# Performance work log

Hardware: AMD Instinct MI355X
Metric: run time of the kernel (lower is better)

## Reference

```python
import jax, jax.numpy as jnp
import numpy as np

N_HEAD, D_HEAD, D_MODEL = 8, 64, 512
QLEN, MLEN, BSZ = 1024, 1024, 4
KLEN = QLEN + MLEN
SCALE = 1.0 / (D_HEAD ** 0.5)
LN_EPS = 1e-5


def _rel_shift(x):
    # x: [qlen, rlen, bsz, n_head]
    q, rl, b, n = x.shape
    zero_pad = jnp.zeros((q, 1, b, n), x.dtype)
    x_padded = jnp.concatenate([zero_pad, x], axis=1).reshape(rl + 1, q, b, n)
    return x_padded[1:].reshape(q, rl, b, n)


def _layer_norm(x, g, b):
    mu = jnp.mean(x, axis=-1, keepdims=True)
    var = jnp.var(x, axis=-1, keepdims=True)
    return (x - mu) * jax.lax.rsqrt(var + LN_EPS) * g + b


def setup_inputs() -> dict:
    key = jax.random.key(0)
    ks = jax.random.split(key, 10)
    s = 0.02
    return {
        "w": jax.random.normal(ks[0], (QLEN, BSZ, D_MODEL), jnp.float32),
        "r": jax.random.normal(ks[1], (KLEN, 1, D_MODEL), jnp.float32),
        "r_w_bias": jax.random.normal(ks[2], (N_HEAD, D_HEAD), jnp.float32) * s,
        "r_r_bias": jax.random.normal(ks[3], (N_HEAD, D_HEAD), jnp.float32) * s,
        "mems": jax.random.normal(ks[4], (MLEN, BSZ, D_MODEL), jnp.float32),
        "Wq": jax.random.normal(ks[5], (D_MODEL, N_HEAD * D_HEAD), jnp.float32) * s,
        "Wkv": jax.random.normal(ks[6], (D_MODEL, 2 * N_HEAD * D_HEAD), jnp.float32) * s,
        "Wr": jax.random.normal(ks[7], (D_MODEL, N_HEAD * D_HEAD), jnp.float32) * s,
        "Wo": jax.random.normal(ks[8], (N_HEAD * D_HEAD, D_MODEL), jnp.float32) * s,
        "ln_g": jnp.ones((D_MODEL,), jnp.float32),
        "ln_b": jnp.zeros((D_MODEL,), jnp.float32),
        # causal mask: query i can attend keys j <= i + MLEN
        "attn_mask": jnp.arange(KLEN)[None, :] > (jnp.arange(QLEN) + MLEN)[:, None],
    }


def reference(w, r, r_w_bias, r_r_bias, mems, Wq, Wkv, Wr, Wo, ln_g, ln_b, attn_mask):
    qlen, bsz = w.shape[0], w.shape[1]
    cat = jnp.concatenate([mems, w], axis=0)          # [klen, bsz, d_model]
    klen = cat.shape[0]

    r_head_k = (r[:, 0] @ Wr).reshape(-1, N_HEAD, D_HEAD)   # [rlen, n, d]
    kv = cat @ Wkv                                           # [klen, bsz, 2*n*d]
    w_head_k, w_head_v = jnp.split(kv, 2, axis=-1)
    w_head_q = (cat[-qlen:] @ Wq).reshape(qlen, bsz, N_HEAD, D_HEAD)
    w_head_k = w_head_k.reshape(klen, bsz, N_HEAD, D_HEAD)
    w_head_v = w_head_v.reshape(klen, bsz, N_HEAD, D_HEAD)

    AC = jnp.einsum('ibnd,jbnd->ijbn', w_head_q + r_w_bias, w_head_k)
    BD = jnp.einsum('ibnd,jnd->ijbn', w_head_q + r_r_bias, r_head_k)
    BD = _rel_shift(BD)[:, :klen]

    attn_score = (AC + BD) * SCALE                           # [qlen, klen, bsz, n]
    attn_score = jnp.where(attn_mask[:, :, None, None], -jnp.inf, attn_score)
    attn_prob = jax.nn.softmax(attn_score, axis=1)

    attn_vec = jnp.einsum('ijbn,jbnd->ibnd', attn_prob, w_head_v)
    attn_vec = attn_vec.reshape(qlen, bsz, N_HEAD * D_HEAD)
    attn_out = attn_vec @ Wo
    return _layer_norm(w + attn_out, ln_g, ln_b)
```

## Files before the change

### kernel.cpp

```cpp
#include <hip/hip_runtime.h>
#include <hip/hip_bf16.h>
#include <math.h>

#define QLEN 1024
#define MLEN 1024
#define KLEN 2048
#define BSZ 4
#define NH 8
#define DH 64
#define DM 512
#define SCALE 0.125f
#define LN_EPS 1e-5f

#define RK_ROWS 2176
#define D2STR 36

typedef __attribute__((ext_vector_type(8))) short short8;
typedef __attribute__((ext_vector_type(4))) float float4_;

__device__ inline ushort to_bf16(float x) {
  __hip_bfloat16 h = __float2bfloat16(x);
  return *reinterpret_cast<ushort*>(&h);
}
__device__ inline float bf16_to_f(ushort u) {
  union { unsigned int i; float f; } v;
  v.i = (unsigned int)u << 16;
  return v.f;
}

__device__ inline float row_max16(float v) {
  int x = __builtin_bit_cast(int, v);
  v = fmaxf(v, __builtin_bit_cast(float, __builtin_amdgcn_update_dpp(x, x, 0xB1, 0xF, 0xF, false)));
  x = __builtin_bit_cast(int, v);
  v = fmaxf(v, __builtin_bit_cast(float, __builtin_amdgcn_update_dpp(x, x, 0x4E, 0xF, 0xF, false)));
  x = __builtin_bit_cast(int, v);
  v = fmaxf(v, __builtin_bit_cast(float, __builtin_amdgcn_update_dpp(x, x, 0x124, 0xF, 0xF, false)));
  x = __builtin_bit_cast(int, v);
  v = fmaxf(v, __builtin_bit_cast(float, __builtin_amdgcn_update_dpp(x, x, 0x128, 0xF, 0xF, false)));
  return v;
}
__device__ inline float row_sum16(float v) {
  int x = __builtin_bit_cast(int, v);
  v += __builtin_bit_cast(float, __builtin_amdgcn_update_dpp(x, x, 0xB1, 0xF, 0xF, false));
  x = __builtin_bit_cast(int, v);
  v += __builtin_bit_cast(float, __builtin_amdgcn_update_dpp(x, x, 0x4E, 0xF, 0xF, false));
  x = __builtin_bit_cast(int, v);
  v += __builtin_bit_cast(float, __builtin_amdgcn_update_dpp(x, x, 0x124, 0xF, 0xF, false));
  x = __builtin_bit_cast(int, v);
  v += __builtin_bit_cast(float, __builtin_amdgcn_update_dpp(x, x, 0x128, 0xF, 0xF, false));
  return v;
}

__global__ __launch_bounds__(256) void wtrans_all(
    const float* __restrict__ Wq, const float* __restrict__ Wkv,
    const float* __restrict__ Wr, const float* __restrict__ Wo,
    ushort* __restrict__ WqT, ushort* __restrict__ WkvT,
    ushort* __restrict__ WrT, ushort* __restrict__ WoT) {
  __shared__ ushort tile[32][33];
  const int z = blockIdx.z;
  const float* W;
  ushort* WT;
  int N;
  if (z == 0)      { W = Wq;  WT = WqT;  N = DM; }
  else if (z == 1) { W = Wkv; WT = WkvT; N = 2 * DM; }
  else if (z == 2) { W = Wr;  WT = WrT;  N = DM; }
  else             { W = Wo;  WT = WoT;  N = DM; }
  const int k0 = blockIdx.x * 32, n0 = blockIdx.y * 32;
  if (n0 >= N) return;
  const int tid = threadIdx.x;
#pragma unroll
  for (int it = 0; it < 4; ++it) {
    int idx = tid + it * 256;
    int r = idx >> 5, c = idx & 31;
    tile[r][c] = to_bf16(W[(size_t)(k0 + r) * N + n0 + c]);
  }
  __syncthreads();
#pragma unroll
  for (int it = 0; it < 4; ++it) {
    int idx = tid + it * 256;
    int r = idx >> 5, c = idx & 31;
    WT[(size_t)(n0 + r) * DM + k0 + c] = tile[c][r];
  }
}

__global__ __launch_bounds__(256) void proj_all(
    const float* __restrict__ w, const float* __restrict__ mems,
    const float* __restrict__ r,
    const ushort* __restrict__ WqT, const ushort* __restrict__ WkvT,
    const ushort* __restrict__ WrT,
    const float* __restrict__ bias0, const float* __restrict__ bias1,
    ushort* __restrict__ qw, ushort* __restrict__ qr,
    ushort* __restrict__ k2, ushort* __restrict__ v2,
    ushort* __restrict__ rk2) {
  __shared__ ushort As[128 * 32];
  __shared__ ushort Bs[128 * 32];
  const int tid = threadIdx.x;
  int mode, bx, by;
  {
    int id = blockIdx.x;
    if (id < 128)      { mode = 0; bx = id >> 2;         by = id & 3; }
    else if (id < 640) { mode = 1; bx = (id - 128) >> 3; by = (id - 128) & 7; }
    else               { mode = 2; bx = (id - 640) >> 2; by = (id - 640) & 3; }
  }
  const int m0 = bx * 128, n0 = by * 128;
  const int wv = tid >> 6, lane = tid & 63;
  const int wm = wv >> 1, wn = wv & 1;
  const int l16 = lane & 15, quad = lane >> 4;

  const int arow = tid >> 1;
  const int acol = (tid & 1) * 16;
  const float* asrc;
  {
    int m = m0 + arow;
    if (mode == 2) asrc = r + (size_t)m * DM;
    else asrc = (m < QLEN * BSZ) ? w + (size_t)m * DM
                                 : mems + (size_t)(m - QLEN * BSZ) * DM;
    asrc += acol;
  }
  const ushort* BT = (mode == 0) ? WqT : (mode == 1) ? WkvT : WrT;
  const ushort* bsrc = BT + (size_t)(n0 + arow) * DM + acol;

  float4_ acc[4][4];
#pragma unroll
  for (int a = 0; a < 4; ++a)
#pragma unroll
    for (int b = 0; b < 4; ++b) acc[a][b] = float4_{0.f, 0.f, 0.f, 0.f};

  for (int k0 = 0; k0 < DM; k0 += 32) {
    float4 a0 = *reinterpret_cast<const float4*>(asrc + k0);
    float4 a1 = *reinterpret_cast<const float4*>(asrc + k0 + 4);
    float4 a2 = *reinterpret_cast<const float4*>(asrc + k0 + 8);
    float4 a3 = *reinterpret_cast<const float4*>(asrc + k0 + 12);
    ushort4 u0, u1, u2, u3;
    u0.x = to_bf16(a0.x); u0.y = to_bf16(a0.y); u0.z = to_bf16(a0.z); u0.w = to_bf16(a0.w);
    u1.x = to_bf16(a1.x); u1.y = to_bf16(a1.y); u1.z = to_bf16(a1.z); u1.w = to_bf16(a1.w);
    u2.x = to_bf16(a2.x); u2.y = to_bf16(a2.y); u2.z = to_bf16(a2.z); u2.w = to_bf16(a2.w);
    u3.x = to_bf16(a3.x); u3.y = to_bf16(a3.y); u3.z = to_bf16(a3.z); u3.w = to_bf16(a3.w);
    *reinterpret_cast<ushort4*>(&As[arow * 32 + acol]) = u0;
    *reinterpret_cast<ushort4*>(&As[arow * 32 + acol + 4]) = u1;
    *reinterpret_cast<ushort4*>(&As[arow * 32 + acol + 8]) = u2;
    *reinterpret_cast<ushort4*>(&As[arow * 32 + acol + 12]) = u3;
    *reinterpret_cast<uint4*>(&Bs[arow * 32 + acol]) =
        *reinterpret_cast<const uint4*>(bsrc + k0);
    *reinterpret_cast<uint4*>(&Bs[arow * 32 + acol + 8]) =
        *reinterpret_cast<const uint4*>(bsrc + k0 + 8);
    __syncthreads();
    short8 af[4], bf[4];
#pragma unroll
    for (int f = 0; f < 4; ++f) {
      af[f] = *reinterpret_cast<const short8*>(&As[(wm * 64 + f * 16 + l16) * 32 + quad * 8]);
      bf[f] = *reinterpret_cast<const short8*>(&Bs[(wn * 64 + f * 16 + l16) * 32 + quad * 8]);
    }
#pragma unroll
    for (int fm = 0; fm < 4; ++fm)
#pragma unroll
      for (int fn = 0; fn < 4; ++fn)
        acc[fm][fn] = __builtin_amdgcn_mfma_f32_16x16x32_bf16(bf[fn], af[fm], acc[fm][fn], 0, 0, 0);
    __syncthreads();
  }

#pragma unroll
  for (int fm = 0; fm < 4; ++fm) {
#pragma unroll
    for (int fn = 0; fn < 4; ++fn) {
      const int mm = m0 + wm * 64 + fm * 16 + l16;
      const int nnb = n0 + wn * 64 + fn * 16 + quad * 4;
      const float4_ a = acc[fm][fn];
      if (mode == 0) {
        float4 b0v = *reinterpret_cast<const float4*>(bias0 + nnb);
        float4 b1v = *reinterpret_cast<const float4*>(bias1 + nnb);
        int i = mm >> 2, b = mm & 3;
        int hd = nnb >> 6, d0 = nnb & 63;
        size_t idx = (((size_t)(b * NH + hd)) * QLEN + i) * DH + d0;
        ushort4 o0, o1;
        o0.x = to_bf16(a[0] + b0v.x); o0.y = to_bf16(a[1] + b0v.y);
        o0.z = to_bf16(a[2] + b0v.z); o0.w = to_bf16(a[3] + b0v.w);
        o1.x = to_bf16(a[0] + b1v.x); o1.y = to_bf16(a[1] + b1v.y);
        o1.z = to_bf16(a[2] + b1v.z); o1.w = to_bf16(a[3] + b1v.w);
        *reinterpret_cast<ushort4*>(qw + idx) = o0;
        *reinterpret_cast<ushort4*>(qr + idx) = o1;
      } else if (mode == 1) {
        int pos = mm >> 2, b = mm & 3;
        if (nnb < DM) {
          int jb = pos >> 5, jj = pos & 31;
          int hd = nnb >> 6, d = nnb & 63;
          int bn = b * NH + hd;
          int tile = ((jj >> 4) << 1) | (d >> 5);
          int lane2 = (((d >> 3) & 3) << 4) | (jj & 15);
          ushort4 o;
          o.x = to_bf16(a[0]); o.y = to_bf16(a[1]);
          o.z = to_bf16(a[2]); o.w = to_bf16(a[3]);
          *reinterpret_cast<ushort4*>(
              k2 + ((((size_t)bn * 64 + jb) * 4 + tile) * 64 + lane2) * 8 + (d & 7)) = o;
        } else {
          int nn2 = nnb - DM;
          int hd = nn2 >> 6, dbase = nn2 & 63;
          int bn = b * NH + hd;
          int jb64 = pos >> 6, j64 = pos & 63;
          int s_g = (j64 & 15) * 4 + (j64 >> 4);
          int half = s_g >> 5, s_ = s_g & 31;
          size_t flat = (((size_t)bn * 32 + jb64) * 8 + (dbase >> 4) * 2 + half) * 512
                      + (size_t)((s_ >> 3) * 16 + (dbase & 15)) * 8 + (s_ & 7);
#pragma unroll
          for (int reg = 0; reg < 4; ++reg)
            v2[flat + (size_t)reg * 8] = to_bf16(a[reg]);
        }
      } else {
        int t = mm;
        int hd = nnb >> 6, d = nnb & 63;
        ushort4 o;
        o.x = to_bf16(a[0]); o.y = to_bf16(a[1]);
        o.z = to_bf16(a[2]); o.w = to_bf16(a[3]);
        *reinterpret_cast<ushort4*>(
            rk2 + ((size_t)hd * RK_ROWS + t) * DH + d) = o;
      }
    }
  }
}

__device__ inline uint4 combine8(uint4 u0, uint4 u1, float s0, float s1) {
  union U { uint4 v; ushort u[8]; };
  U a, b, o;
  a.v = u0; b.v = u1;
#pragma unroll
  for (int e = 0; e < 8; ++e)
    o.u[e] = to_bf16(bf16_to_f(a.u[e]) * s0 + bf16_to_f(b.u[e]) * s1);
  return o.v;
}

__global__ __launch_bounds__(256) void mfma_out(
    const ushort* __restrict__ O0, const ushort* __restrict__ O1,
    const float* __restrict__ ml, const ushort* __restrict__ BT,
    float* __restrict__ Y) {
  __shared__ ushort As[128 * 32];
  __shared__ ushort Bs[128 * 32];
  const int tid = threadIdx.x;
  const int m0 = blockIdx.x * 128, n0 = blockIdx.y * 128;
  const int wv = tid >> 6, lane = tid & 63;
  const int wm = wv >> 1, wn = wv & 1;
  const int l16 = lane & 15, quad = lane >> 4;
  const int arow = tid >> 1;
  const int acol = (tid & 1) * 16;
  const int row = m0 + arow;
  const ushort* bsrc = BT + (size_t)(n0 + arow) * DM + acol;
  const float2* mlp = (const float2*)ml;

  float4_ acc[4][4];
#pragma unroll
  for (int a = 0; a < 4; ++a)
#pragma unroll
    for (int b = 0; b < 4; ++b) acc[a][b] = float4_{0.f, 0.f, 0.f, 0.f};

  for (int k0 = 0; k0 < DM; k0 += 32) {
    const int col0 = k0 + acol;
    const int h = col0 >> 6;
    float2 a = mlp[(size_t)row * NH + h];
    float2 c = mlp[(size_t)(QLEN * BSZ + row) * NH + h];
    float M = fmaxf(a.x, c.x);
    float e0 = __builtin_amdgcn_exp2f(a.x - M);
    float e1 = __builtin_amdgcn_exp2f(c.x - M);
    float inv = 1.f / (a.y * e0 + c.y * e1);
    float s0 = e0 * inv, s1 = e1 * inv;
    size_t ob = (size_t)row * DM + col0;
    uint4 u0a = *reinterpret_cast<const uint4*>(O0 + ob);
    uint4 u0b = *reinterpret_cast<const uint4*>(O0 + ob + 8);
    uint4 u1a = *reinterpret_cast<const uint4*>(O1 + ob);
    uint4 u1b = *reinterpret_cast<const uint4*>(O1 + ob + 8);
    *reinterpret_cast<uint4*>(&As[arow * 32 + acol]) = combine8(u0a, u1a, s0, s1);
    *reinterpret_cast<uint4*>(&As[arow * 32 + acol + 8]) = combine8(u0b, u1b, s0, s1);
    *reinterpret_cast<uint4*>(&Bs[arow * 32 + acol]) = *reinterpret_cast<const uint4*>(bsrc + k0);
    *reinterpret_cast<uint4*>(&Bs[arow * 32 + acol + 8]) = *reinterpret_cast<const uint4*>(bsrc + k0 + 8);
    __syncthreads();
    short8 af[4], bf[4];
#pragma unroll
    for (int f = 0; f < 4; ++f) {
      af[f] = *reinterpret_cast<const short8*>(&As[(wm * 64 + f * 16 + l16) * 32 + quad * 8]);
      bf[f] = *reinterpret_cast<const short8*>(&Bs[(wn * 64 + f * 16 + l16) * 32 + quad * 8]);
    }
#pragma unroll
    for (int fm = 0; fm < 4; ++fm)
#pragma unroll
      for (int fn = 0; fn < 4; ++fn)
        acc[fm][fn] = __builtin_amdgcn_mfma_f32_16x16x32_bf16(bf[fn], af[fm], acc[fm][fn], 0, 0, 0);
    __syncthreads();
  }
#pragma unroll
  for (int fm = 0; fm < 4; ++fm)
#pragma unroll
    for (int fn = 0; fn < 4; ++fn) {
      int mm = m0 + wm * 64 + fm * 16 + l16;
      int nnb = n0 + wn * 64 + fn * 16 + quad * 4;
      float4 o;
      o.x = acc[fm][fn][0]; o.y = acc[fm][fn][1];
      o.z = acc[fm][fn][2]; o.w = acc[fm][fn][3];
      *reinterpret_cast<float4*>(Y + (size_t)mm * DM + nnb) = o;
    }
}

__global__ __launch_bounds__(256) void ln_fuse(
    const float* __restrict__ y, const float* __restrict__ wres,
    const float* __restrict__ g, const float* __restrict__ bb,
    float* __restrict__ out) {
  const int row = blockIdx.x * 4 + (threadIdx.x >> 6);
  const int lane = threadIdx.x & 63;
  const float* yr = y + (size_t)row * DM + lane * 4;
  const float* wr = wres + (size_t)row * DM + lane * 4;
  float4 x0 = *(const float4*)yr;
  float4 x1 = *(const float4*)(yr + 256);
  float4 w0 = *(const float4*)wr;
  float4 w1 = *(const float4*)(wr + 256);
  x0.x += w0.x; x0.y += w0.y; x0.z += w0.z; x0.w += w0.w;
  x1.x += w1.x; x1.y += w1.y; x1.z += w1.z; x1.w += w1.w;
  float s = x0.x + x0.y + x0.z + x0.w + x1.x + x1.y + x1.z + x1.w;
  float ss = x0.x * x0.x + x0.y * x0.y + x0.z * x0.z + x0.w * x0.w +
             x1.x * x1.x + x1.y * x1.y + x1.z * x1.z + x1.w * x1.w;
#pragma unroll
  for (int off = 1; off <= 32; off <<= 1) {
    s += __shfl_xor(s, off, 64);
    ss += __shfl_xor(ss, off, 64);
  }
  float mu = s * (1.f / DM);
  float var = ss * (1.f / DM) - mu * mu;
  float rstd = rsqrtf(var + LN_EPS);
  float4 g0 = *(const float4*)(g + lane * 4);
  float4 g1 = *(const float4*)(g + lane * 4 + 256);
  float4 b0 = *(const float4*)(bb + lane * 4);
  float4 b1 = *(const float4*)(bb + lane * 4 + 256);
  float4 o0, o1;
  o0.x = (x0.x - mu) * rstd * g0.x + b0.x;
  o0.y = (x0.y - mu) * rstd * g0.y + b0.y;
  o0.z = (x0.z - mu) * rstd * g0.z + b0.z;
  o0.w = (x0.w - mu) * rstd * g0.w + b0.w;
  o1.x = (x1.x - mu) * rstd * g1.x + b1.x;
  o1.y = (x1.y - mu) * rstd * g1.y + b1.y;
  o1.z = (x1.z - mu) * rstd * g1.z + b1.z;
  o1.w = (x1.w - mu) * rstd * g1.w + b1.w;
  float* orow = out + (size_t)row * DM + lane * 4;
  *reinterpret_cast<float4*>(orow) = o0;
  *reinterpret_cast<float4*>(orow + 256) = o1;
}

__global__ __launch_bounds__(256, 2) void attn_mfma(
    const ushort* __restrict__ qw, const ushort* __restrict__ qr,
    const ushort* __restrict__ k2, const ushort* __restrict__ v2,
    const ushort* __restrict__ rk2, ushort* __restrict__ Opart,
    float* __restrict__ ml) {
  const int i0b = (gridDim.x - 1 - blockIdx.x) * 128;
  const int n = blockIdx.y;
  const int b = blockIdx.z >> 1, seg = blockIdx.z & 1;
  const int bn = b * NH + n;
  const int tid = threadIdx.x;
  const int wv = tid >> 6, lane = tid & 63;
  const int l16 = lane & 15, quad = lane >> 4;
  const int i0w = i0b + wv * 32;

  __shared__ float D2all[4][96 * D2STR];
  __shared__ ushort Pall[4][1024];
  float* __restrict__ Dw = D2all[wv];
  ushort* __restrict__ Pw = Pall[wv];

  const ushort* __restrict__ k2b = k2 + (size_t)bn * (64 * 4 * 512);
  const ushort* __restrict__ v2b = v2 + (size_t)bn * (32 * 8 * 512);
  const ushort* __restrict__ rk2n = rk2 + (size_t)n * RK_ROWS * DH;

  const int nIterTot = i0b / 64 + 18;
  const int nHalf = nIterTot >> 1;
  const int c0 = seg ? nHalf : 0;
  const int c1 = seg ? nIterTot : nHalf;

  short8 aqw[2][2], aqr[2][2];
#pragma unroll
  for (int g = 0; g < 2; ++g) {
    const ushort* qwp = qw + (((size_t)bn * QLEN) + i0w + g * 16 + l16) * DH + quad * 8;
    const ushort* qrp = qr + (((size_t)bn * QLEN) + i0w + g * 16 + l16) * DH + quad * 8;
    aqw[g][0] = *(const short8*)(qwp);
    aqw[g][1] = *(const short8*)(qwp + 32);
    aqr[g][0] = *(const short8*)(qrp);
    aqr[g][1] = *(const short8*)(qrp + 32);
  }

  float4_ O[2][4];
  float mrow[2][4], lpart[2][4];
#pragma unroll
  for (int g = 0; g < 2; ++g)
#pragma unroll
    for (int t = 0; t < 4; ++t) {
      O[g][t] = float4_{0.f, 0.f, 0.f, 0.f};
      mrow[g][t] = -INFINITY;
      lpart[g][t] = 0.f;
    }
  const float SL2E = SCALE * 1.44269504088896f;

  for (int k = c0; k < c1; ++k) {
    const int j0 = k * 64;

    float4_ ac[2][4];
#pragma unroll
    for (int h = 0; h < 4; ++h) {
      const ushort* kb = k2b +
          ((size_t)(k * 2 + (h >> 1)) * 4 + (h & 1) * 2) * 512 + lane * 8;
      short8 b0 = *(const short8*)(kb);
      short8 b1 = *(const short8*)(kb + 512);
#pragma unroll
      for (int g = 0; g < 2; ++g) {
        float4_ c = {0.f, 0.f, 0.f, 0.f};
        c = __builtin_amdgcn_mfma_f32_16x16x32_bf16(aqw[g][0], b0, c, 0, 0, 0);
        c = __builtin_amdgcn_mfma_f32_16x16x32_bf16(aqw[g][1], b1, c, 0, 0, 0);
        ac[g][h] = c;
      }
    }

    const int rb = j0 - i0w + 992;
#pragma unroll
    for (int tt = 0; tt < 6; ++tt) {
      const ushort* rrow = rk2n + (size_t)(rb + tt * 16 + l16) * DH;
      short8 r0 = *(const short8*)(rrow + quad * 8);
      short8 r1 = *(const short8*)(rrow + 32 + quad * 8);
      float* dst = Dw + (tt * 16 + l16) * D2STR + quad * 4;
      if (tt < 5) {
        float4_ d = {0.f, 0.f, 0.f, 0.f};
        d = __builtin_amdgcn_mfma_f32_16x16x32_bf16(aqr[1][0], r0, d, 0, 0, 0);
        d = __builtin_amdgcn_mfma_f32_16x16x32_bf16(aqr[1][1], r1, d, 0, 0, 0);
        *reinterpret_cast<float4_*>(dst + 16) = d;
      }
      if (tt > 0) {
        float4_ d = {0.f, 0.f, 0.f, 0.f};
        d = __builtin_amdgcn_mfma_f32_16x16x32_bf16(aqr[0][0], r0, d, 0, 0, 0);
        d = __builtin_amdgcn_mfma_f32_16x16x32_bf16(aqr[0][1], r1, d, 0, 0, 0);
        *reinterpret_cast<float4_*>(dst) = d;
      }
    }

    short8 pf[2][2];
#pragma unroll
    for (int g = 0; g < 2; ++g) {
      float s4[4][4];
#pragma unroll
      for (int hh = 0; hh < 4; ++hh)
#pragma unroll
        for (int rg = 0; rg < 4; ++rg) {
          int wrow = g * 16 + quad * 4 + rg;
          float bd = Dw[(hh * 16 + l16 + 31 - wrow) * D2STR + wrow];
          float sv = (ac[g][hh][rg] + bd) * SL2E;
          s4[hh][rg] = (j0 + hh * 16 + l16 > i0w + wrow + MLEN) ? -INFINITY : sv;
        }
#pragma unroll
      for (int rg = 0; rg < 4; ++rg) {
        float mx = row_max16(fmaxf(fmaxf(s4[0][rg], s4[1][rg]),
                                   fmaxf(s4[2][rg], s4[3][rg])));
        float mn = fmaxf(mrow[g][rg], mx);
        float alpha = __builtin_amdgcn_exp2f(mrow[g][rg] - mn);
        float p0 = __builtin_amdgcn_exp2f(s4[0][rg] - mn);
        float p1 = __builtin_amdgcn_exp2f(s4[1][rg] - mn);
        float p2 = __builtin_amdgcn_exp2f(s4[2][rg] - mn);
        float p3 = __builtin_amdgcn_exp2f(s4[3][rg] - mn);
        lpart[g][rg] = lpart[g][rg] * alpha + (p0 + p1 + p2 + p3);
        mrow[g][rg] = mn;
#pragma unroll
        for (int t = 0; t < 4; ++t) O[g][t][rg] *= alpha;
        unsigned int u0 = (unsigned int)to_bf16(p0) | ((unsigned int)to_bf16(p1) << 16);
        unsigned int u1 = (unsigned int)to_bf16(p2) | ((unsigned int)to_bf16(p3) << 16);
        int flat = (l16 >> 1) * 128 + (quad * 4 + rg) * 8 + (l16 & 1) * 4;
        *reinterpret_cast<uint2*>(Pw + flat) = make_uint2(u0, u1);
      }
      pf[g][0] = *(const short8*)(Pw + lane * 8);
      pf[g][1] = *(const short8*)(Pw + 512 + lane * 8);
    }

#pragma unroll
    for (int t = 0; t < 4; ++t) {
      const ushort* vb = v2b + ((size_t)k * 8 + t * 2) * 512 + lane * 8;
      short8 vf0 = *(const short8*)(vb);
      short8 vf1 = *(const short8*)(vb + 512);
#pragma unroll
      for (int g = 0; g < 2; ++g) {
        O[g][t] = __builtin_amdgcn_mfma_f32_16x16x32_bf16(pf[g][0], vf0, O[g][t], 0, 0, 0);
        O[g][t] = __builtin_amdgcn_mfma_f32_16x16x32_bf16(pf[g][1], vf1, O[g][t], 0, 0, 0);
      }
    }
  }

  ushort* op = Opart + (size_t)seg * QLEN * BSZ * DM;
  float2* mlp = (float2*)ml;
#pragma unroll
  for (int g = 0; g < 2; ++g) {
    float lsum[4];
#pragma unroll
    for (int rg = 0; rg < 4; ++rg) lsum[rg] = row_sum16(lpart[g][rg]);
#pragma unroll
    for (int rg = 0; rg < 4; ++rg) {
      int row = g * 16 + quad * 4 + rg;
      if (l16 == 0) {
        mlp[((size_t)seg * QLEN * BSZ + (size_t)(i0w + row) * BSZ + b) * NH + n] =
            float2{mrow[g][rg], lsum[rg]};
      }
#pragma unroll
      for (int t = 0; t < 4; ++t) {
        op[((size_t)(i0w + row) * BSZ + b) * DM + n * DH + t * 16 + l16] =
            to_bf16(O[g][t][rg]);
      }
    }
  }
}

extern "C" void kernel_launch(void* const* d_in, const int* in_sizes, int n_in,
                              void* d_out, int out_size, void* d_ws, size_t ws_size,
                              hipStream_t stream) {
  const float* w    = (const float*)d_in[0];
  const float* r    = (const float*)d_in[1];
  const float* rwb  = (const float*)d_in[2];
  const float* rrb  = (const float*)d_in[3];
  const float* mems = (const float*)d_in[4];
  const float* Wq   = (const float*)d_in[5];
  const float* Wkv  = (const float*)d_in[6];
  const float* Wr   = (const float*)d_in[7];
  const float* Wo   = (const float*)d_in[8];
  const float* ln_g = (const float*)d_in[9];
  const float* ln_b = (const float*)d_in[10];
  float* out = (float*)d_out;

  char* p = (char*)d_ws;
  auto alloc = [&](size_t bytes) {
    char* q = p;
    p += (bytes + 255) & ~(size_t)255;
    return q;
  };
  ushort* WqT   = (ushort*)alloc((size_t)DM * DM * 2);
  ushort* WkvT  = (ushort*)alloc((size_t)2 * DM * DM * 2);
  ushort* WrT   = (ushort*)alloc((size_t)DM * DM * 2);
  ushort* WoT   = (ushort*)alloc((size_t)DM * DM * 2);
  ushort* qw    = (ushort*)alloc((size_t)BSZ * NH * QLEN * DH * 2);
  ushort* qr    = (ushort*)alloc((size_t)BSZ * NH * QLEN * DH * 2);
  ushort* k2    = (ushort*)alloc((size_t)BSZ * NH * 64 * 4 * 512 * 2);
  ushort* v2    = (ushort*)alloc((size_t)BSZ * NH * 32 * 8 * 512 * 2);
  ushort* rk2   = (ushort*)alloc((size_t)NH * RK_ROWS * DH * 2);
  ushort* Opart = (ushort*)alloc((size_t)2 * QLEN * BSZ * DM * 2);
  float*  ml    = (float*)alloc((size_t)2 * QLEN * BSZ * NH * 2 * 4);
  float* y = (float*)k2;

  wtrans_all<<<dim3(16, 32, 4), dim3(256), 0, stream>>>(
      Wq, Wkv, Wr, Wo, WqT, WkvT, WrT, WoT);
  proj_all<<<dim3(704), dim3(256), 0, stream>>>(
      w, mems, r, WqT, WkvT, WrT, rwb, rrb, qw, qr, k2, v2, rk2);
  attn_mfma<<<dim3(QLEN / 128, NH, BSZ * 2), dim3(256), 0, stream>>>(
      qw, qr, k2, v2, rk2, Opart, ml);
  mfma_out<<<dim3(32, 4), dim3(256), 0, stream>>>(
      Opart, Opart + (size_t)QLEN * BSZ * DM, ml, WoT, y);
  ln_fuse<<<dim3(QLEN * BSZ / 4), dim3(256), 0, stream>>>(y, w, ln_g, ln_b, out);
}
```

Baseline: 258.8 us.

## Prefetch K/V fragments, store BD in bf16, swizzle P buffer, add MFMA priorities

Next-iteration K fragments are now loaded into registers while the current iteration computes, and V fragments are loaded at the start of each iteration so global latency overlaps the MFMA and softmax work. The relative-position BD scratch tile in LDS is stored as bf16 instead of fp32, which halves its LDS footprint and traffic. The P staging buffer uses an XOR-swizzled layout to reduce LDS bank conflicts. s_setprio is raised around MFMA blocks. The changes add register pressure that may hurt occupancy, and the bf16 BD scratch adds rounding error.

```diff
diff --git a/kernel.cpp b/kernel.cpp
--- a/kernel.cpp
+++ b/kernel.cpp
@@ -354,9 +354,9 @@
   const int l16 = lane & 15, quad = lane >> 4;
   const int i0w = i0b + wv * 32;
 
-  __shared__ float D2all[4][96 * D2STR];
+  __shared__ ushort D2all[4][96 * D2STR];
   __shared__ ushort Pall[4][1024];
-  float* __restrict__ Dw = D2all[wv];
+  ushort* __restrict__ Dw = D2all[wv];
   ushort* __restrict__ Pw = Pall[wv];
 
   const ushort* __restrict__ k2b = k2 + (size_t)bn * (64 * 4 * 512);
@@ -390,46 +390,78 @@
       lpart[g][t] = 0.f;
     }
   const float SL2E = SCALE * 1.44269504088896f;
+  const int px = l16 >> 1, ppar = l16 & 1;
+
+  short8 kf[8], kfN[8];
+  auto load_k = [&](int kk, short8* dst) {
+#pragma unroll
+    for (int h = 0; h < 4; ++h) {
+      const ushort* kb = k2b +
+          ((size_t)(kk * 2 + (h >> 1)) * 4 + (h & 1) * 2) * 512 + lane * 8;
+      dst[h * 2 + 0] = *(const short8*)(kb);
+      dst[h * 2 + 1] = *(const short8*)(kb + 512);
+    }
+  };
+  load_k(c0, kf);
 
   for (int k = c0; k < c1; ++k) {
     const int j0 = k * 64;
 
+    short8 vf[8];
+#pragma unroll
+    for (int t = 0; t < 4; ++t) {
+      const ushort* vb = v2b + ((size_t)k * 8 + t * 2) * 512 + lane * 8;
+      vf[t * 2 + 0] = *(const short8*)(vb);
+      vf[t * 2 + 1] = *(const short8*)(vb + 512);
+    }
+
+    __builtin_amdgcn_s_setprio(1);
     float4_ ac[2][4];
 #pragma unroll
     for (int h = 0; h < 4; ++h) {
-      const ushort* kb = k2b +
-          ((size_t)(k * 2 + (h >> 1)) * 4 + (h & 1) * 2) * 512 + lane * 8;
-      short8 b0 = *(const short8*)(kb);
-      short8 b1 = *(const short8*)(kb + 512);
 #pragma unroll
       for (int g = 0; g < 2; ++g) {
         float4_ c = {0.f, 0.f, 0.f, 0.f};
-        c = __builtin_amdgcn_mfma_f32_16x16x32_bf16(aqw[g][0], b0, c, 0, 0, 0);
-        c = __builtin_amdgcn_mfma_f32_16x16x32_bf16(aqw[g][1], b1, c, 0, 0, 0);
+        c = __builtin_amdgcn_mfma_f32_16x16x32_bf16(aqw[g][0], kf[h * 2], c, 0, 0, 0);
+        c = __builtin_amdgcn_mfma_f32_16x16x32_bf16(aqw[g][1], kf[h * 2 + 1], c, 0, 0, 0);
         ac[g][h] = c;
       }
     }
+    __builtin_amdgcn_s_setprio(0);
+
+    {
+      int kn = k + 1; if (kn > c1 - 1) kn = c1 - 1;
+      load_k(kn, kfN);
+    }
 
     const int rb = j0 - i0w + 992;
+    __builtin_amdgcn_s_setprio(1);
 #pragma unroll
     for (int tt = 0; tt < 6; ++tt) {
       const ushort* rrow = rk2n + (size_t)(rb + tt * 16 + l16) * DH;
       short8 r0 = *(const short8*)(rrow + quad * 8);
       short8 r1 = *(const short8*)(rrow + 32 + quad * 8);
-      float* dst = Dw + (tt * 16 + l16) * D2STR + quad * 4;
+      ushort* dst = Dw + (tt * 16 + l16) * D2STR + quad * 4;
       if (tt < 5) {
         float4_ d = {0.f, 0.f, 0.f, 0.f};
         d = __builtin_amdgcn_mfma_f32_16x16x32_bf16(aqr[1][0], r0, d, 0, 0, 0);
         d = __builtin_amdgcn_mfma_f32_16x16x32_bf16(aqr[1][1], r1, d, 0, 0, 0);
-        *reinterpret_cast<float4_*>(dst + 16) = d;
+        ushort4 du;
+        du.x = to_bf16(d[0]); du.y = to_bf16(d[1]);
+        du.z = to_bf16(d[2]); du.w = to_bf16(d[3]);
+        *reinterpret_cast<ushort4*>(dst + 16) = du;
       }
       if (tt > 0) {
         float4_ d = {0.f, 0.f, 0.f, 0.f};
         d = __builtin_amdgcn_mfma_f32_16x16x32_bf16(aqr[0][0], r0, d, 0, 0, 0);
         d = __builtin_amdgcn_mfma_f32_16x16x32_bf16(aqr[0][1], r1, d, 0, 0, 0);
-        *reinterpret_cast<float4_*>(dst) = d;
-      }
-    }
+        ushort4 du;
+        du.x = to_bf16(d[0]); du.y = to_bf16(d[1]);
+        du.z = to_bf16(d[2]); du.w = to_bf16(d[3]);
+        *reinterpret_cast<ushort4*>(dst) = du;
+      }
+    }
+    __builtin_amdgcn_s_setprio(0);
 
     short8 pf[2][2];
 #pragma unroll
@@ -440,7 +472,7 @@
 #pragma unroll
         for (int rg = 0; rg < 4; ++rg) {
           int wrow = g * 16 + quad * 4 + rg;
-          float bd = Dw[(hh * 16 + l16 + 31 - wrow) * D2STR + wrow];
+          float bd = bf16_to_f(Dw[(hh * 16 + l16 + 31 - wrow) * D2STR + wrow]);
           float sv = (ac[g][hh][rg] + bd) * SL2E;
           s4[hh][rg] = (j0 + hh * 16 + l16 > i0w + wrow + MLEN) ? -INFINITY : sv;
         }
@@ -460,24 +492,27 @@
         for (int t = 0; t < 4; ++t) O[g][t][rg] *= alpha;
         unsigned int u0 = (unsigned int)to_bf16(p0) | ((unsigned int)to_bf16(p1) << 16);
         unsigned int u1 = (unsigned int)to_bf16(p2) | ((unsigned int)to_bf16(p3) << 16);
-        int flat = (l16 >> 1) * 128 + (quad * 4 + rg) * 8 + (l16 & 1) * 4;
-        *reinterpret_cast<uint2*>(Pw + flat) = make_uint2(u0, u1);
-      }
-      pf[g][0] = *(const short8*)(Pw + lane * 8);
-      pf[g][1] = *(const short8*)(Pw + 512 + lane * 8);
-    }
-
+        int row = quad * 4 + rg;
+        int off = px * 128 + ((row ^ px)) * 8 + ppar * 4;
+        *reinterpret_cast<uint2*>(Pw + off) = make_uint2(u0, u1);
+      }
+      pf[g][0] = *(const short8*)(Pw + quad * 128 + (l16 ^ quad) * 8);
+      pf[g][1] = *(const short8*)(Pw + 512 + quad * 128 + (l16 ^ (quad + 4)) * 8);
+    }
+
+    __builtin_amdgcn_s_setprio(1);
 #pragma unroll
     for (int t = 0; t < 4; ++t) {
-      const ushort* vb = v2b + ((size_t)k * 8 + t * 2) * 512 + lane * 8;
-      short8 vf0 = *(const short8*)(vb);
-      short8 vf1 = *(const short8*)(vb + 512);
 #pragma unroll
       for (int g = 0; g < 2; ++g) {
-        O[g][t] = __builtin_amdgcn_mfma_f32_16x16x32_bf16(pf[g][0], vf0, O[g][t], 0, 0, 0);
-        O[g][t] = __builtin_amdgcn_mfma_f32_16x16x32_bf16(pf[g][1], vf1, O[g][t], 0, 0, 0);
-      }
-    }
+        O[g][t] = __builtin_amdgcn_mfma_f32_16x16x32_bf16(pf[g][0], vf[t * 2], O[g][t], 0, 0, 0);
+        O[g][t] = __builtin_amdgcn_mfma_f32_16x16x32_bf16(pf[g][1], vf[t * 2 + 1], O[g][t], 0, 0, 0);
+      }
+    }
+    __builtin_amdgcn_s_setprio(0);
+
+#pragma unroll
+    for (int h = 0; h < 8; ++h) kf[h] = kfN[h];
   }
 
   ushort* op = Opart + (size_t)seg * QLEN * BSZ * DM;
```

After: 256.4 us. About the same (-0.9%).
